# Optimization experiments

Hardware: AMD Instinct MI355X
Metric: run time of the kernel (lower is better)

Reference implementation:

```python
import jax, jax.numpy as jnp
import numpy as np

B, N, C = 8, 4096, 1024
ATT_DIM = 512
M = 64  # num_outputs


def setup_inputs() -> dict:
    key = jax.random.key(0)
    k_x, k_w, k_b, k_av = jax.random.split(key, 4)
    x = jax.random.normal(k_x, (B, N, C), dtype=jnp.float32)
    # nn.Linear(input_dim, attention_dim): weight (att, C), bias (att,)
    lim = 1.0 / np.sqrt(C)
    W = jax.random.uniform(k_w, (ATT_DIM, C), dtype=jnp.float32, minval=-lim, maxval=lim)
    b = jax.random.uniform(k_b, (ATT_DIM,), dtype=jnp.float32, minval=-lim, maxval=lim)
    # torch.rand -> uniform [0,1)
    attention_vectors = jax.random.uniform(k_av, (M, ATT_DIM), dtype=jnp.float32)
    return {"x": x, "W": W, "b": b, "attention_vectors": attention_vectors}


def reference(x, W, b, attention_vectors):
    # linear projection: (B,N,C) @ (C,att) + bias -> (B,N,att)
    scores = jnp.einsum('bnc,dc->bnd', x, W) + b
    # learned-query attention logits: (B,M,N)
    logits = jnp.einsum('bnd,md->bmn', scores, attention_vectors)
    weights = jax.nn.softmax(logits, axis=-1)
    # pool original features: (B,M,N) @ (B,N,C) -> (B,M,C)
    return jnp.einsum('bmn,bnc->bmc', weights, x)
```

## Files before the change

kernel.cpp:

```cpp
#include <hip/hip_runtime.h>
#include <hip/hip_bf16.h>

#define Bn 8
#define Nn 4096
#define Cn 1024
#define Dn 512
#define Mn 64

typedef __hip_bfloat16 bf16;
typedef __attribute__((ext_vector_type(8))) short short8;
typedef __attribute__((ext_vector_type(4))) short short4x;
typedef __attribute__((ext_vector_type(4))) float f32x4;

#define MFMA16(a, b, c) __builtin_amdgcn_mfma_f32_16x16x32_bf16((a), (b), (c), 0, 0, 0)

__device__ inline short bfbits(float f) {
  union { bf16 b; short s; } u;
  u.b = __float2bfloat16(f);
  return u.s;
}

__global__ __launch_bounds__(256) void prep_kernel(
    const float* __restrict__ W, const float* __restrict__ bias,
    const float* __restrict__ av, bf16* __restrict__ Vhi,
    bf16* __restrict__ Vlo, float* __restrict__ c0) {
  const int m = blockIdx.x;
  const int t = threadIdx.x;
  const int cl = t & 63, dg = t >> 6;
  const int c = blockIdx.y * 64 + cl;
  const float* wp = W + (size_t)(dg * 128) * Cn + c;
  const float* ap = av + m * Dn + dg * 128;
  float a0 = 0.f, a1 = 0.f, a2 = 0.f, a3 = 0.f;
#pragma unroll 8
  for (int i = 0; i < 128; i += 4) {
    a0 = fmaf(ap[i + 0], wp[(size_t)(i + 0) * Cn], a0);
    a1 = fmaf(ap[i + 1], wp[(size_t)(i + 1) * Cn], a1);
    a2 = fmaf(ap[i + 2], wp[(size_t)(i + 2) * Cn], a2);
    a3 = fmaf(ap[i + 3], wp[(size_t)(i + 3) * Cn], a3);
  }
  __shared__ float red[256];
  red[t] = (a0 + a1) + (a2 + a3);
  __syncthreads();
  const float v = red[cl] + red[cl + 64] + red[cl + 128] + red[cl + 192];
  if (dg == 0) {
    const bf16 hi = __float2bfloat16(v);
    Vhi[m * Cn + c] = hi;
    Vlo[m * Cn + c] = __float2bfloat16(v - __bfloat162float(hi));
  }
  if (blockIdx.y == 0) {
    __syncthreads();
    red[t] = av[m * Dn + t] * bias[t] + av[m * Dn + t + 256] * bias[t + 256];
    __syncthreads();
    if (t < 64) {
      float s = red[t] + red[t + 64] + red[t + 128] + red[t + 192];
#pragma unroll
      for (int off = 32; off > 0; off >>= 1) s += __shfl_down(s, off);
      if (t == 0) c0[m] = s;
    }
  }
}

__global__ __launch_bounds__(256) void logits_sm_kernel(
    const float* __restrict__ x, const bf16* __restrict__ Vhi,
    const bf16* __restrict__ Vlo, const float* __restrict__ c0,
    bf16* __restrict__ wgt, float* __restrict__ Mp, float* __restrict__ Sp) {
  const int g = blockIdx.x;
  const int n0 = g * 64;
  const int b = blockIdx.y;
  const int t = threadIdx.x;
  __shared__ short Xs[64][136];
  __shared__ short VsH[64][136];
  __shared__ short VsL[64][136];
  const int w = t >> 6, lane = t & 63, lr = lane & 15, q = lane >> 4;
  const ptrdiff_t dlo = Vlo - Vhi;

  int ur[4], uc[4];
  const float* xsrc[4];
  const bf16* hsrc[4];
#pragma unroll
  for (int j = 0; j < 4; ++j) {
    const int u = t + 256 * j;
    ur[j] = u >> 4;
    uc[j] = (u & 15) * 8;
    xsrc[j] = x + (size_t)(b * Nn + n0 + ur[j]) * Cn + uc[j];
    hsrc[j] = Vhi + ur[j] * Cn + uc[j];
  }

  f32x4 acc[4];
#pragma unroll
  for (int i = 0; i < 4; ++i) acc[i] = (f32x4){0.f, 0.f, 0.f, 0.f};

  float4 px0[4], px1[4];
  short8 pvh[4], pvl[4];
#pragma unroll
  for (int j = 0; j < 4; ++j) {
    px0[j] = *(const float4*)(xsrc[j]);
    px1[j] = *(const float4*)(xsrc[j] + 4);
    pvh[j] = *(const short8*)(hsrc[j]);
    pvl[j] = *(const short8*)(hsrc[j] + dlo);
  }

  for (int k0 = 0; k0 < Cn; k0 += 128) {
#pragma unroll
    for (int j = 0; j < 4; ++j) {
      short8 s;
      s[0] = bfbits(px0[j].x); s[1] = bfbits(px0[j].y);
      s[2] = bfbits(px0[j].z); s[3] = bfbits(px0[j].w);
      s[4] = bfbits(px1[j].x); s[5] = bfbits(px1[j].y);
      s[6] = bfbits(px1[j].z); s[7] = bfbits(px1[j].w);
      *(short8*)&Xs[ur[j]][uc[j]] = s;
      *(short8*)&VsH[ur[j]][uc[j]] = pvh[j];
      *(short8*)&VsL[ur[j]][uc[j]] = pvl[j];
    }
    __syncthreads();
    if (k0 + 128 < Cn) {
#pragma unroll
      for (int j = 0; j < 4; ++j) {
        px0[j] = *(const float4*)(xsrc[j] + k0 + 128);
        px1[j] = *(const float4*)(xsrc[j] + k0 + 132);
        pvh[j] = *(const short8*)(hsrc[j] + k0 + 128);
        pvl[j] = *(const short8*)(hsrc[j] + dlo + k0 + 128);
      }
    }
#pragma unroll
    for (int kk = 0; kk < 128; kk += 32) {
      const short8 a = *(const short8*)&Xs[w * 16 + lr][kk + q * 8];
#pragma unroll
      for (int mt = 0; mt < 4; ++mt) {
        acc[mt] = MFMA16(a, *(const short8*)&VsH[mt * 16 + lr][kk + q * 8], acc[mt]);
        acc[mt] = MFMA16(a, *(const short8*)&VsL[mt * 16 + lr][kk + q * 8], acc[mt]);
      }
    }
    __syncthreads();
  }

  float* wredM = (float*)&Xs[0][0];
  float* wredS = wredM + 256;
  float rmax[4];
#pragma unroll
  for (int mt = 0; mt < 4; ++mt) {
    float r = fmaxf(fmaxf(acc[mt][0], acc[mt][1]), fmaxf(acc[mt][2], acc[mt][3]));
    r = fmaxf(r, __shfl_xor(r, 16));
    r = fmaxf(r, __shfl_xor(r, 32));
    rmax[mt] = r;
  }
  if (q == 0)
#pragma unroll
    for (int mt = 0; mt < 4; ++mt) wredM[w * 64 + mt * 16 + lr] = rmax[mt];
  __syncthreads();
  float vv[4][4];
#pragma unroll
  for (int mt = 0; mt < 4; ++mt) {
    const int m = mt * 16 + lr;
    const float mp = fmaxf(fmaxf(wredM[m], wredM[64 + m]),
                           fmaxf(wredM[128 + m], wredM[192 + m]));
    float s = 0.f;
#pragma unroll
    for (int r = 0; r < 4; ++r) {
      vv[mt][r] = __expf(acc[mt][r] - mp);
      s += vv[mt][r];
    }
    s += __shfl_xor(s, 16);
    s += __shfl_xor(s, 32);
    if (q == 0) wredS[w * 64 + m] = s;
  }
#pragma unroll
  for (int mt = 0; mt < 4; ++mt) {
    const int m = mt * 16 + lr;
    short4x o;
    o[0] = bfbits(vv[mt][0]); o[1] = bfbits(vv[mt][1]);
    o[2] = bfbits(vv[mt][2]); o[3] = bfbits(vv[mt][3]);
    *(short4x*)&wgt[(size_t)(b * Mn + m) * Nn + n0 + w * 16 + q * 4] = o;
  }
  __syncthreads();
  if (w == 0) {
    const int m = lane;
    const float mp = fmaxf(fmaxf(wredM[m], wredM[64 + m]),
                           fmaxf(wredM[128 + m], wredM[192 + m]));
    const float sp = wredS[m] + wredS[64 + m] + wredS[128 + m] + wredS[192 + m];
    Mp[((size_t)b * Mn + m) * 64 + g] = mp + c0[m];
    Sp[((size_t)b * Mn + m) * 64 + g] = sp;
  }
}

__global__ __launch_bounds__(256) void pool_kernel(
    const float* __restrict__ x, const bf16* __restrict__ wgt,
    const float* __restrict__ Mp, const float* __restrict__ Sp,
    float* __restrict__ part) {
  const int cbase = blockIdx.x * 64;
  const int b = blockIdx.y;
  const int ks = blockIdx.z;
  const int t = threadIdx.x;
  __shared__ short XT[64][136];
  __shared__ float scs[16][64];
  const int w = t >> 6, lane = t & 63, lr = lane & 15, q = lane >> 4;
  const int mh = (w & 1) * 32, ch = (w >> 1) * 32;

  {
    const int m = t >> 2, qq = t & 3;
    const float* mpp = Mp + ((size_t)b * Mn + m) * 64 + qq * 16;
    const float* spp = Sp + ((size_t)b * Mn + m) * 64 + qq * 16;
    float mpl[16], spl[16];
#pragma unroll
    for (int j = 0; j < 16; ++j) { mpl[j] = mpp[j]; spl[j] = spp[j]; }
    float lmax = -3.4e38f;
#pragma unroll
    for (int j = 0; j < 16; ++j) lmax = fmaxf(lmax, mpl[j]);
    float gmax = fmaxf(lmax, __shfl_xor(lmax, 1));
    gmax = fmaxf(gmax, __shfl_xor(gmax, 2));
    float lsum = 0.f;
#pragma unroll
    for (int j = 0; j < 16; ++j) lsum += __expf(mpl[j] - gmax) * spl[j];
    float gsum = lsum + __shfl_xor(lsum, 1);
    gsum = gsum + __shfl_xor(gsum, 2);
    if (qq == ks) {
      const float inv = 1.f / gsum;
#pragma unroll
      for (int j = 0; j < 16; ++j) scs[j][m] = __expf(mpl[j] - gmax) * inv;
    }
  }
  __syncthreads();

  f32x4 accT[2][2], accg[2][2];
#pragma unroll
  for (int i = 0; i < 2; ++i)
#pragma unroll
    for (int j = 0; j < 2; ++j) {
      accT[i][j] = (f32x4){0.f, 0.f, 0.f, 0.f};
      accg[i][j] = (f32x4){0.f, 0.f, 0.f, 0.f};
    }

  const int h = t & 15, g = t >> 4;
  const int swz = 8 * (h & 7);
  const int swzr0 = 8 * (((ch + lr) >> 2) & 7);
  const int swzr1 = 8 * (((ch + 16 + lr) >> 2) & 7);
  const int NQ = Nn / 4;
  const int kbase = ks * NQ;
  const float* xsrc = x + (size_t)b * Nn * Cn + (size_t)(kbase + 4 * g) * Cn + cbase + 4 * h;
  const bf16* wr0 = wgt + (size_t)(b * Mn + mh + lr) * Nn + kbase;
  const bf16* wr1 = wr0 + (size_t)16 * Nn;

  float4 pf[8];
#pragma unroll
  for (int i = 0; i < 4; ++i) {
    pf[i]     = *(const float4*)(xsrc + (size_t)i * Cn);
    pf[4 + i] = *(const float4*)(xsrc + (size_t)(64 + i) * Cn);
  }

  for (int kc = 0; kc < NQ; kc += 128) {
#pragma unroll
    for (int blk = 0; blk < 2; ++blk) {
      const float4 r0 = pf[blk * 4 + 0], r1 = pf[blk * 4 + 1];
      const float4 r2 = pf[blk * 4 + 2], r3 = pf[blk * 4 + 3];
      const int kof = (blk * 64 + 4 * g) ^ swz;
      short4x v0, v1, v2, v3;
      v0[0] = bfbits(r0.x); v0[1] = bfbits(r1.x); v0[2] = bfbits(r2.x); v0[3] = bfbits(r3.x);
      v1[0] = bfbits(r0.y); v1[1] = bfbits(r1.y); v1[2] = bfbits(r2.y); v1[3] = bfbits(r3.y);
      v2[0] = bfbits(r0.z); v2[1] = bfbits(r1.z); v2[2] = bfbits(r2.z); v2[3] = bfbits(r3.z);
      v3[0] = bfbits(r0.w); v3[1] = bfbits(r1.w); v3[2] = bfbits(r2.w); v3[3] = bfbits(r3.w);
      *(short4x*)&XT[4 * h + 0][kof] = v0;
      *(short4x*)&XT[4 * h + 1][kof] = v1;
      *(short4x*)&XT[4 * h + 2][kof] = v2;
      *(short4x*)&XT[4 * h + 3][kof] = v3;
    }
    __syncthreads();
    if (kc + 128 < NQ) {
#pragma unroll
      for (int i = 0; i < 4; ++i) {
        pf[i]     = *(const float4*)(xsrc + (size_t)(kc + 128 + i) * Cn);
        pf[4 + i] = *(const float4*)(xsrc + (size_t)(kc + 192 + i) * Cn);
      }
    }
#pragma unroll
    for (int kk = 0; kk < 128; kk += 32) {
      const short8 a0 = *(const short8*)(wr0 + kc + kk + q * 8);
      const short8 a1 = *(const short8*)(wr1 + kc + kk + q * 8);
      const short8 b0 = *(const short8*)&XT[ch + lr][(kk + q * 8) ^ swzr0];
      const short8 b1 = *(const short8*)&XT[ch + 16 + lr][(kk + q * 8) ^ swzr1];
      accg[0][0] = MFMA16(a0, b0, accg[0][0]);
      accg[0][1] = MFMA16(a0, b1, accg[0][1]);
      accg[1][0] = MFMA16(a1, b0, accg[1][0]);
      accg[1][1] = MFMA16(a1, b1, accg[1][1]);
      if (kk == 32 || kk == 96) {
        const int gl = (kc + kk) >> 6;
#pragma unroll
        for (int mi = 0; mi < 2; ++mi)
#pragma unroll
          for (int r = 0; r < 4; ++r) {
            const float s = scs[gl][mh + mi * 16 + q * 4 + r];
            accT[mi][0][r] = fmaf(s, accg[mi][0][r], accT[mi][0][r]);
            accT[mi][1][r] = fmaf(s, accg[mi][1][r], accT[mi][1][r]);
            accg[mi][0][r] = 0.f;
            accg[mi][1][r] = 0.f;
          }
      }
    }
    __syncthreads();
  }
  float* pout = part + ((size_t)ks * Bn + b) * Mn * Cn;
#pragma unroll
  for (int mi = 0; mi < 2; ++mi)
#pragma unroll
    for (int ci = 0; ci < 2; ++ci) {
      const int m = mh + mi * 16 + q * 4;
      const int c = cbase + ch + ci * 16 + lr;
#pragma unroll
      for (int reg = 0; reg < 4; ++reg)
        pout[(size_t)(m + reg) * Cn + c] = accT[mi][ci][reg];
    }
}

__global__ __launch_bounds__(256) void reduce_kernel(
    const float* __restrict__ part, float* __restrict__ out) {
  const int i = blockIdx.x * 256 + threadIdx.x;
  const float4* p = (const float4*)part;
  const int S4 = (Bn * Mn * Cn) / 4;
  const float4 v0 = p[i], v1 = p[i + S4], v2 = p[i + 2 * S4], v3 = p[i + 3 * S4];
  float4 o;
  o.x = (v0.x + v1.x) + (v2.x + v3.x);
  o.y = (v0.y + v1.y) + (v2.y + v3.y);
  o.z = (v0.z + v1.z) + (v2.z + v3.z);
  o.w = (v0.w + v1.w) + (v2.w + v3.w);
  ((float4*)out)[i] = o;
}

extern "C" void kernel_launch(void* const* d_in, const int* in_sizes, int n_in,
                              void* d_out, int out_size, void* d_ws, size_t ws_size,
                              hipStream_t stream) {
  const float* x = (const float*)d_in[0];
  const float* W = (const float*)d_in[1];
  const float* bias = (const float*)d_in[2];
  const float* av = (const float*)d_in[3];
  float* out = (float*)d_out;
  char* ws = (char*)d_ws;

  bf16* Vhi = (bf16*)(ws + 0);
  bf16* Vlo = (bf16*)(ws + 131072);
  float* c0 = (float*)(ws + 262144);
  bf16* wgt = (bf16*)(ws + 263168);
  float* Mp = (float*)(ws + 4457472);
  float* Sp = (float*)(ws + 4588544);
  float* part = (float*)(ws + 4719616);

  prep_kernel<<<dim3(Mn, Cn / 64), 256, 0, stream>>>(W, bias, av, Vhi, Vlo, c0);
  logits_sm_kernel<<<dim3(Nn / 64, Bn), 256, 0, stream>>>(x, Vhi, Vlo, c0, wgt, Mp, Sp);
  pool_kernel<<<dim3(Cn / 64, Bn, 4), 256, 0, stream>>>(x, wgt, Mp, Sp, part);
  reduce_kernel<<<(Bn * Mn * Cn) / 1024, 256, 0, stream>>>(part, out);
}
```

Before: 261.6 us.

## Restructure logits, softmax normalization, pooling split-K and LDS double buffering

The logits kernel drops LDS staging and reads x into a three-deep register prefetch pipeline. It reads the V hi/lo operands straight from global memory and L2, and asks for two blocks per CU. A new norm kernel rescales the bf16 weights in place with the global softmax factors. This removes the per-group rescale fix-ups inside the pool kernel. The pool kernel now double-buffers its transposed-x LDS tile, drops one barrier per step, and splits K eight ways instead of four. The reduce kernel is widened to match, which doubles the partial-sum workspace and adds one launch.

```diff
diff --git a/kernel.cpp b/kernel.cpp
--- a/kernel.cpp
+++ b/kernel.cpp
@@ -18,6 +18,11 @@
   union { bf16 b; short s; } u;
   u.b = __float2bfloat16(f);
   return u.s;
+}
+__device__ inline float bfval(short s) {
+  union { short s; bf16 b; } u;
+  u.s = s;
+  return __bfloat162float(u.b);
 }
 
 __global__ __launch_bounds__(256) void prep_kernel(
@@ -60,7 +65,7 @@
   }
 }
 
-__global__ __launch_bounds__(256) void logits_sm_kernel(
+__global__ __launch_bounds__(256, 2) void logits_sm_kernel(
     const float* __restrict__ x, const bf16* __restrict__ Vhi,
     const bf16* __restrict__ Vlo, const float* __restrict__ c0,
     bf16* __restrict__ wgt, float* __restrict__ Mp, float* __restrict__ Sp) {
@@ -68,74 +73,57 @@
   const int n0 = g * 64;
   const int b = blockIdx.y;
   const int t = threadIdx.x;
-  __shared__ short Xs[64][136];
-  __shared__ short VsH[64][136];
-  __shared__ short VsL[64][136];
   const int w = t >> 6, lane = t & 63, lr = lane & 15, q = lane >> 4;
-  const ptrdiff_t dlo = Vlo - Vhi;
-
-  int ur[4], uc[4];
-  const float* xsrc[4];
-  const bf16* hsrc[4];
-#pragma unroll
-  for (int j = 0; j < 4; ++j) {
-    const int u = t + 256 * j;
-    ur[j] = u >> 4;
-    uc[j] = (u & 15) * 8;
-    xsrc[j] = x + (size_t)(b * Nn + n0 + ur[j]) * Cn + uc[j];
-    hsrc[j] = Vhi + ur[j] * Cn + uc[j];
-  }
+
+  const float* xrow = x + (size_t)(b * Nn + n0 + w * 16 + lr) * Cn + q * 8;
+  const bf16* vh = Vhi + (size_t)lr * Cn + q * 8;
+  const bf16* vl = Vlo + (size_t)lr * Cn + q * 8;
 
   f32x4 acc[4];
 #pragma unroll
   for (int i = 0; i < 4; ++i) acc[i] = (f32x4){0.f, 0.f, 0.f, 0.f};
 
-  float4 px0[4], px1[4];
-  short8 pvh[4], pvl[4];
-#pragma unroll
-  for (int j = 0; j < 4; ++j) {
-    px0[j] = *(const float4*)(xsrc[j]);
-    px1[j] = *(const float4*)(xsrc[j] + 4);
-    pvh[j] = *(const short8*)(hsrc[j]);
-    pvl[j] = *(const short8*)(hsrc[j] + dlo);
-  }
-
-  for (int k0 = 0; k0 < Cn; k0 += 128) {
-#pragma unroll
-    for (int j = 0; j < 4; ++j) {
-      short8 s;
-      s[0] = bfbits(px0[j].x); s[1] = bfbits(px0[j].y);
-      s[2] = bfbits(px0[j].z); s[3] = bfbits(px0[j].w);
-      s[4] = bfbits(px1[j].x); s[5] = bfbits(px1[j].y);
-      s[6] = bfbits(px1[j].z); s[7] = bfbits(px1[j].w);
-      *(short8*)&Xs[ur[j]][uc[j]] = s;
-      *(short8*)&VsH[ur[j]][uc[j]] = pvh[j];
-      *(short8*)&VsL[ur[j]][uc[j]] = pvl[j];
-    }
-    __syncthreads();
-    if (k0 + 128 < Cn) {
-#pragma unroll
-      for (int j = 0; j < 4; ++j) {
-        px0[j] = *(const float4*)(xsrc[j] + k0 + 128);
-        px1[j] = *(const float4*)(xsrc[j] + k0 + 132);
-        pvh[j] = *(const short8*)(hsrc[j] + k0 + 128);
-        pvl[j] = *(const short8*)(hsrc[j] + dlo + k0 + 128);
+  float4 xa0[4], xa1[4], xb0[4], xb1[4], xc0[4], xc1[4];
+#pragma unroll
+  for (int s = 0; s < 4; ++s) {
+    xa0[s] = *(const float4*)(xrow + s * 32);
+    xa1[s] = *(const float4*)(xrow + s * 32 + 4);
+    xb0[s] = *(const float4*)(xrow + 128 + s * 32);
+    xb1[s] = *(const float4*)(xrow + 128 + s * 32 + 4);
+    xc0[s] = xb0[s]; xc1[s] = xb1[s];
+  }
+
+  for (int kc = 0; kc < Cn; kc += 128) {
+    if (kc + 256 < Cn) {
+#pragma unroll
+      for (int s = 0; s < 4; ++s) {
+        xc0[s] = *(const float4*)(xrow + kc + 256 + s * 32);
+        xc1[s] = *(const float4*)(xrow + kc + 256 + s * 32 + 4);
       }
     }
 #pragma unroll
-    for (int kk = 0; kk < 128; kk += 32) {
-      const short8 a = *(const short8*)&Xs[w * 16 + lr][kk + q * 8];
+    for (int s = 0; s < 4; ++s) {
+      const int kk = kc + s * 32;
+      short8 a;
+      a[0] = bfbits(xa0[s].x); a[1] = bfbits(xa0[s].y);
+      a[2] = bfbits(xa0[s].z); a[3] = bfbits(xa0[s].w);
+      a[4] = bfbits(xa1[s].x); a[5] = bfbits(xa1[s].y);
+      a[6] = bfbits(xa1[s].z); a[7] = bfbits(xa1[s].w);
 #pragma unroll
       for (int mt = 0; mt < 4; ++mt) {
-        acc[mt] = MFMA16(a, *(const short8*)&VsH[mt * 16 + lr][kk + q * 8], acc[mt]);
-        acc[mt] = MFMA16(a, *(const short8*)&VsL[mt * 16 + lr][kk + q * 8], acc[mt]);
+        acc[mt] = MFMA16(a, *(const short8*)(vh + (size_t)(mt * 16) * Cn + kk), acc[mt]);
+        acc[mt] = MFMA16(a, *(const short8*)(vl + (size_t)(mt * 16) * Cn + kk), acc[mt]);
       }
     }
-    __syncthreads();
-  }
-
-  float* wredM = (float*)&Xs[0][0];
-  float* wredS = wredM + 256;
+#pragma unroll
+    for (int s = 0; s < 4; ++s) {
+      xa0[s] = xb0[s]; xa1[s] = xb1[s];
+      xb0[s] = xc0[s]; xb1[s] = xc1[s];
+    }
+  }
+
+  __shared__ float wredM[256];
+  __shared__ float wredS[256];
   float rmax[4];
 #pragma unroll
   for (int mt = 0; mt < 4; ++mt) {
@@ -183,58 +171,60 @@
   }
 }
 
-__global__ __launch_bounds__(256) void pool_kernel(
+__global__ __launch_bounds__(256) void norm_kernel(
+    bf16* __restrict__ wgt, const float* __restrict__ Mp,
+    const float* __restrict__ Sp) {
+  const int row = blockIdx.x;
+  const int t = threadIdx.x;
+  __shared__ float sMS[2];
+  if (t < 64) {
+    const float mp = Mp[(size_t)row * 64 + t];
+    const float sp = Sp[(size_t)row * 64 + t];
+    float M = mp;
+#pragma unroll
+    for (int off = 32; off > 0; off >>= 1) M = fmaxf(M, __shfl_xor(M, off));
+    float e = __expf(mp - M) * sp;
+#pragma unroll
+    for (int off = 32; off > 0; off >>= 1) e += __shfl_xor(e, off);
+    if (t == 0) { sMS[0] = M; sMS[1] = e; }
+  }
+  __syncthreads();
+  const float M = sMS[0], inv = 1.f / sMS[1];
+  const float sc = __expf(Mp[(size_t)row * 64 + (t >> 2)] - M) * inv;
+  bf16* wp = wgt + (size_t)row * Nn + t * 16;
+  short8 u0 = *(const short8*)(wp);
+  short8 u1 = *(const short8*)(wp + 8);
+  short8 o0, o1;
+#pragma unroll
+  for (int j = 0; j < 8; ++j) {
+    o0[j] = bfbits(bfval(u0[j]) * sc);
+    o1[j] = bfbits(bfval(u1[j]) * sc);
+  }
+  *(short8*)(wp) = o0;
+  *(short8*)(wp + 8) = o1;
+}
+
+__global__ __launch_bounds__(256, 4) void pool_kernel(
     const float* __restrict__ x, const bf16* __restrict__ wgt,
-    const float* __restrict__ Mp, const float* __restrict__ Sp,
     float* __restrict__ part) {
   const int cbase = blockIdx.x * 64;
   const int b = blockIdx.y;
   const int ks = blockIdx.z;
   const int t = threadIdx.x;
-  __shared__ short XT[64][136];
-  __shared__ float scs[16][64];
+  __shared__ short XT[2][64][136];
   const int w = t >> 6, lane = t & 63, lr = lane & 15, q = lane >> 4;
   const int mh = (w & 1) * 32, ch = (w >> 1) * 32;
-
-  {
-    const int m = t >> 2, qq = t & 3;
-    const float* mpp = Mp + ((size_t)b * Mn + m) * 64 + qq * 16;
-    const float* spp = Sp + ((size_t)b * Mn + m) * 64 + qq * 16;
-    float mpl[16], spl[16];
-#pragma unroll
-    for (int j = 0; j < 16; ++j) { mpl[j] = mpp[j]; spl[j] = spp[j]; }
-    float lmax = -3.4e38f;
-#pragma unroll
-    for (int j = 0; j < 16; ++j) lmax = fmaxf(lmax, mpl[j]);
-    float gmax = fmaxf(lmax, __shfl_xor(lmax, 1));
-    gmax = fmaxf(gmax, __shfl_xor(gmax, 2));
-    float lsum = 0.f;
-#pragma unroll
-    for (int j = 0; j < 16; ++j) lsum += __expf(mpl[j] - gmax) * spl[j];
-    float gsum = lsum + __shfl_xor(lsum, 1);
-    gsum = gsum + __shfl_xor(gsum, 2);
-    if (qq == ks) {
-      const float inv = 1.f / gsum;
-#pragma unroll
-      for (int j = 0; j < 16; ++j) scs[j][m] = __expf(mpl[j] - gmax) * inv;
-    }
-  }
-  __syncthreads();
-
-  f32x4 accT[2][2], accg[2][2];
+  f32x4 acc[2][2];
 #pragma unroll
   for (int i = 0; i < 2; ++i)
 #pragma unroll
-    for (int j = 0; j < 2; ++j) {
-      accT[i][j] = (f32x4){0.f, 0.f, 0.f, 0.f};
-      accg[i][j] = (f32x4){0.f, 0.f, 0.f, 0.f};
-    }
+    for (int j = 0; j < 2; ++j) acc[i][j] = (f32x4){0.f, 0.f, 0.f, 0.f};
 
   const int h = t & 15, g = t >> 4;
   const int swz = 8 * (h & 7);
   const int swzr0 = 8 * (((ch + lr) >> 2) & 7);
   const int swzr1 = 8 * (((ch + 16 + lr) >> 2) & 7);
-  const int NQ = Nn / 4;
+  const int NQ = Nn / 8;
   const int kbase = ks * NQ;
   const float* xsrc = x + (size_t)b * Nn * Cn + (size_t)(kbase + 4 * g) * Cn + cbase + 4 * h;
   const bf16* wr0 = wgt + (size_t)(b * Mn + mh + lr) * Nn + kbase;
@@ -246,56 +236,65 @@
     pf[i]     = *(const float4*)(xsrc + (size_t)i * Cn);
     pf[4 + i] = *(const float4*)(xsrc + (size_t)(64 + i) * Cn);
   }
-
-  for (int kc = 0; kc < NQ; kc += 128) {
-#pragma unroll
-    for (int blk = 0; blk < 2; ++blk) {
-      const float4 r0 = pf[blk * 4 + 0], r1 = pf[blk * 4 + 1];
-      const float4 r2 = pf[blk * 4 + 2], r3 = pf[blk * 4 + 3];
-      const int kof = (blk * 64 + 4 * g) ^ swz;
-      short4x v0, v1, v2, v3;
-      v0[0] = bfbits(r0.x); v0[1] = bfbits(r1.x); v0[2] = bfbits(r2.x); v0[3] = bfbits(r3.x);
-      v1[0] = bfbits(r0.y); v1[1] = bfbits(r1.y); v1[2] = bfbits(r2.y); v1[3] = bfbits(r3.y);
-      v2[0] = bfbits(r0.z); v2[1] = bfbits(r1.z); v2[2] = bfbits(r2.z); v2[3] = bfbits(r3.z);
-      v3[0] = bfbits(r0.w); v3[1] = bfbits(r1.w); v3[2] = bfbits(r2.w); v3[3] = bfbits(r3.w);
-      *(short4x*)&XT[4 * h + 0][kof] = v0;
-      *(short4x*)&XT[4 * h + 1][kof] = v1;
-      *(short4x*)&XT[4 * h + 2][kof] = v2;
-      *(short4x*)&XT[4 * h + 3][kof] = v3;
-    }
+#pragma unroll
+  for (int blk = 0; blk < 2; ++blk) {
+    const float4 r0 = pf[blk * 4 + 0], r1 = pf[blk * 4 + 1];
+    const float4 r2 = pf[blk * 4 + 2], r3 = pf[blk * 4 + 3];
+    const int kof = (blk * 64 + 4 * g) ^ swz;
+    short4x v0, v1, v2, v3;
+    v0[0] = bfbits(r0.x); v0[1] = bfbits(r1.x); v0[2] = bfbits(r2.x); v0[3] = bfbits(r3.x);
+    v1[0] = bfbits(r0.y); v1[1] = bfbits(r1.y); v1[2] = bfbits(r2.y); v1[3] = bfbits(r3.y);
+    v2[0] = bfbits(r0.z); v2[1] = bfbits(r1.z); v2[2] = bfbits(r2.z); v2[3] = bfbits(r3.z);
+    v3[0] = bfbits(r0.w); v3[1] = bfbits(r1.w); v3[2] = bfbits(r2.w); v3[3] = bfbits(r3.w);
+    *(short4x*)&XT[0][4 * h + 0][kof] = v0;
+    *(short4x*)&XT[0][4 * h + 1][kof] = v1;
+    *(short4x*)&XT[0][4 * h + 2][kof] = v2;
+    *(short4x*)&XT[0][4 * h + 3][kof] = v3;
+  }
+#pragma unroll
+  for (int i = 0; i < 4; ++i) {
+    pf[i]     = *(const float4*)(xsrc + (size_t)(128 + i) * Cn);
+    pf[4 + i] = *(const float4*)(xsrc + (size_t)(192 + i) * Cn);
+  }
+
+  int cur = 0;
+  for (int kc = 0; kc < NQ; kc += 128, cur ^= 1) {
     __syncthreads();
     if (kc + 128 < NQ) {
 #pragma unroll
-      for (int i = 0; i < 4; ++i) {
-        pf[i]     = *(const float4*)(xsrc + (size_t)(kc + 128 + i) * Cn);
-        pf[4 + i] = *(const float4*)(xsrc + (size_t)(kc + 192 + i) * Cn);
+      for (int blk = 0; blk < 2; ++blk) {
+        const float4 r0 = pf[blk * 4 + 0], r1 = pf[blk * 4 + 1];
+        const float4 r2 = pf[blk * 4 + 2], r3 = pf[blk * 4 + 3];
+        const int kof = (blk * 64 + 4 * g) ^ swz;
+        short4x v0, v1, v2, v3;
+        v0[0] = bfbits(r0.x); v0[1] = bfbits(r1.x); v0[2] = bfbits(r2.x); v0[3] = bfbits(r3.x);
+        v1[0] = bfbits(r0.y); v1[1] = bfbits(r1.y); v1[2] = bfbits(r2.y); v1[3] = bfbits(r3.y);
+        v2[0] = bfbits(r0.z); v2[1] = bfbits(r1.z); v2[2] = bfbits(r2.z); v2[3] = bfbits(r3.z);
+        v3[0] = bfbits(r0.w); v3[1] = bfbits(r1.w); v3[2] = bfbits(r2.w); v3[3] = bfbits(r3.w);
+        *(short4x*)&XT[cur ^ 1][4 * h + 0][kof] = v0;
+        *(short4x*)&XT[cur ^ 1][4 * h + 1][kof] = v1;
+        *(short4x*)&XT[cur ^ 1][4 * h + 2][kof] = v2;
+        *(short4x*)&XT[cur ^ 1][4 * h + 3][kof] = v3;
+      }
+      if (kc + 256 < NQ) {
+#pragma unroll
+        for (int i = 0; i < 4; ++i) {
+          pf[i]     = *(const float4*)(xsrc + (size_t)(kc + 256 + i) * Cn);
+          pf[4 + i] = *(const float4*)(xsrc + (size_t)(kc + 320 + i) * Cn);
+        }
       }
     }
 #pragma unroll
     for (int kk = 0; kk < 128; kk += 32) {
       const short8 a0 = *(const short8*)(wr0 + kc + kk + q * 8);
       const short8 a1 = *(const short8*)(wr1 + kc + kk + q * 8);
-      const short8 b0 = *(const short8*)&XT[ch + lr][(kk + q * 8) ^ swzr0];
-      const short8 b1 = *(const short8*)&XT[ch + 16 + lr][(kk + q * 8) ^ swzr1];
-      accg[0][0] = MFMA16(a0, b0, accg[0][0]);
-      accg[0][1] = MFMA16(a0, b1, accg[0][1]);
-      accg[1][0] = MFMA16(a1, b0, accg[1][0]);
-      accg[1][1] = MFMA16(a1, b1, accg[1][1]);
-      if (kk == 32 || kk == 96) {
-        const int gl = (kc + kk) >> 6;
-#pragma unroll
-        for (int mi = 0; mi < 2; ++mi)
-#pragma unroll
-          for (int r = 0; r < 4; ++r) {
-            const float s = scs[gl][mh + mi * 16 + q * 4 + r];
-            accT[mi][0][r] = fmaf(s, accg[mi][0][r], accT[mi][0][r]);
-            accT[mi][1][r] = fmaf(s, accg[mi][1][r], accT[mi][1][r]);
-            accg[mi][0][r] = 0.f;
-            accg[mi][1][r] = 0.f;
-          }
-      }
-    }
-    __syncthreads();
+      const short8 b0 = *(const short8*)&XT[cur][ch + lr][(kk + q * 8) ^ swzr0];
+      const short8 b1 = *(const short8*)&XT[cur][ch + 16 + lr][(kk + q * 8) ^ swzr1];
+      acc[0][0] = MFMA16(a0, b0, acc[0][0]);
+      acc[0][1] = MFMA16(a0, b1, acc[0][1]);
+      acc[1][0] = MFMA16(a1, b0, acc[1][0]);
+      acc[1][1] = MFMA16(a1, b1, acc[1][1]);
+    }
   }
   float* pout = part + ((size_t)ks * Bn + b) * Mn * Cn;
 #pragma unroll
@@ -306,7 +305,7 @@
       const int c = cbase + ch + ci * 16 + lr;
 #pragma unroll
       for (int reg = 0; reg < 4; ++reg)
-        pout[(size_t)(m + reg) * Cn + c] = accT[mi][ci][reg];
+        pout[(size_t)(m + reg) * Cn + c] = acc[mi][ci][reg];
     }
 }
 
@@ -315,12 +314,12 @@
   const int i = blockIdx.x * 256 + threadIdx.x;
   const float4* p = (const float4*)part;
   const int S4 = (Bn * Mn * Cn) / 4;
-  const float4 v0 = p[i], v1 = p[i + S4], v2 = p[i + 2 * S4], v3 = p[i + 3 * S4];
-  float4 o;
-  o.x = (v0.x + v1.x) + (v2.x + v3.x);
-  o.y = (v0.y + v1.y) + (v2.y + v3.y);
-  o.z = (v0.z + v1.z) + (v2.z + v3.z);
-  o.w = (v0.w + v1.w) + (v2.w + v3.w);
+  float4 o = (float4){0.f, 0.f, 0.f, 0.f};
+#pragma unroll
+  for (int j = 0; j < 8; ++j) {
+    const float4 v = p[i + j * S4];
+    o.x += v.x; o.y += v.y; o.z += v.z; o.w += v.w;
+  }
   ((float4*)out)[i] = o;
 }
 
@@ -344,6 +343,7 @@
 
   prep_kernel<<<dim3(Mn, Cn / 64), 256, 0, stream>>>(W, bias, av, Vhi, Vlo, c0);
   logits_sm_kernel<<<dim3(Nn / 64, Bn), 256, 0, stream>>>(x, Vhi, Vlo, c0, wgt, Mp, Sp);
-  pool_kernel<<<dim3(Cn / 64, Bn, 4), 256, 0, stream>>>(x, wgt, Mp, Sp, part);
+  norm_kernel<<<Bn * Mn, 256, 0, stream>>>(wgt, Mp, Sp);
+  pool_kernel<<<dim3(Cn / 64, Bn, 8), 256, 0, stream>>>(x, wgt, part);
   reduce_kernel<<<(Bn * Mn * Cn) / 1024, 256, 0, stream>>>(part, out);
 }
```

New measurement: 289.7 us. 10.8% more time.
